# Optimization experiments

Measured on AMD Instinct MI355X. Metric: run time of the kernel, lower is better.

The kernel has to match this reference:

```python
import jax, jax.numpy as jnp
import numpy as np
from jax import lax

B, M, L = 4, 20, 200
IN_C, C1, C2 = 2048, 512, 256
CDIM, DC1, DC2, SDIM = 300, 512, 256, 1024
NEG = -1e15  # -INFINITY in source


def conv1d(x, w, b, pad):
    # x: [N, Cin, L], w: [Cout, Cin, K]
    y = lax.conv_general_dilated(x, w, (1,), ((pad, pad),),
                                 dimension_numbers=('NCH', 'OIH', 'NCH'))
    return y + b[None, :, None]


def maxpool2(x):
    return lax.reduce_window(x, -jnp.inf, lax.max, (1, 1, 2), (1, 1, 2), 'VALID')


def deconv1d(x, w, b):
    # torch ConvTranspose1d(k=4, s=2, p=1): conv with lhs_dilation=2, pad k-1-p=2,
    # kernel flipped and in/out swapped. w: [Cin, Cout, K]
    wt = jnp.flip(w, -1).transpose(1, 0, 2)  # [Cout, Cin, K]
    y = lax.conv_general_dilated(x, wt, (1,), ((2, 2),), lhs_dilation=(2,),
                                 dimension_numbers=('NCH', 'OIH', 'NCH'))
    return y + b[None, :, None]


def setup_inputs() -> dict:
    key = jax.random.key(0)
    ks = jax.random.split(key, 16)
    p = lambda k, sh, s=0.02: (jax.random.normal(k, sh, jnp.float32) * s)
    return dict(
        batch=jax.random.normal(ks[0], (B, M, L, IN_C), jnp.float32),
        seg_len=jax.random.randint(ks[1], (B, M), 1, L + 1, jnp.int32),
        concept1=jax.random.normal(ks[2], (B, CDIM), jnp.float32),
        concept2=jax.random.normal(ks[3], (B, CDIM), jnp.float32),
        w_conv1=p(ks[4], (C1, IN_C, 5)), b_conv1=jnp.zeros((C1,), jnp.float32),
        w_conv2=p(ks[5], (C2, C1, 5)), b_conv2=jnp.zeros((C2,), jnp.float32),
        w_ca1=p(ks[6], (C2, CDIM)), w_ca2=p(ks[7], (C2, C2)), w_ca3=p(ks[8], (1, C2)),
        w_dc1=p(ks[9], (3 * C2, DC1, 4)), b_dc1=jnp.zeros((DC1,), jnp.float32),
        w_dc2=p(ks[10], (DC1, DC2, 4)), b_dc2=jnp.zeros((DC2,), jnp.float32),
        w_sim1=p(ks[11], (SDIM, DC2)), w_sim2=p(ks[12], (SDIM, CDIM)),
        w_mlp=p(ks[13], (1, SDIM)), b_mlp=jnp.zeros((1,), jnp.float32),
    )


def reference(batch, seg_len, concept1, concept2,
              w_conv1, b_conv1, w_conv2, b_conv2,
              w_ca1, w_ca2, w_ca3,
              w_dc1, b_dc1, w_dc2, b_dc2,
              w_sim1, w_sim2, w_mlp, b_mlp):
    Bs, Ms, Ls = batch.shape[:3]
    Lq = Ls // 4
    x = batch.reshape(Bs * Ms, Ls, -1).transpose(0, 2, 1)        # [BM, IN_C, L]
    t1 = maxpool2(conv1d(x, w_conv1, b_conv1, 2))                # [BM, C1, L/2]
    t2 = maxpool2(conv1d(t1, w_conv2, b_conv2, 2)).transpose(0, 2, 1)  # [BM, L/4, C2]

    # vectorized ragged mask: k < ceil(seg_len/4)
    mask = (jnp.arange(Lq)[None, None, :] < ((seg_len + 3) // 4)[:, :, None])
    mask = mask.reshape(Bs * Ms, Lq)

    kproj = t2 @ w_ca2.T                                         # [BM, Lq, C2]

    def concept_att(concept):
        # additive attention; scores are identical across the query-frame dim,
        # so compute one row and broadcast the weighted sum.
        q = concept @ w_ca1.T                                    # [B, C2]
        qe = jnp.repeat(q, Ms, axis=0)                           # [BM, C2]
        s = jnp.tanh(qe[:, None, :] + kproj) @ w_ca3[0]          # [BM, Lq]
        s = jnp.where(mask, s, NEG)
        a = jax.nn.softmax(s, axis=-1)
        r = jnp.einsum('bk,bkc->bc', a, t2)                      # [BM, C2]
        return jnp.broadcast_to(r[:, None, :], t2.shape)         # [BM, Lq, C2]

    r1 = concept_att(concept1)
    r2 = concept_att(concept2)

    cat = jnp.concatenate([t2, r1, r2], axis=-1).transpose(0, 2, 1)  # [BM, 3C2, Lq]
    d = deconv1d(cat, w_dc1, b_dc1)                              # [BM, DC1, L/2]
    d = deconv1d(d, w_dc2, b_dc2).transpose(0, 2, 1)             # [BM, L, DC2]
    d = d.reshape(Bs, Ms * Ls, -1)

    sim1 = d @ w_sim1.T                                          # [B, M*L, SDIM]
    c1 = concept1 @ w_sim2.T                                     # [B, SDIM]
    c2 = concept2 @ w_sim2.T
    sc1 = jax.nn.sigmoid((c1[:, None, :] * sim1) @ w_mlp[0] + b_mlp[0])
    sc2 = jax.nn.sigmoid((c2[:, None, :] * sim1) @ w_mlp[0] + b_mlp[0])
    return sc1.reshape(Bs, Ms, Ls), sc2.reshape(Bs, Ms, Ls)
```

## Files before the change

### kernel.cpp

```cpp
#include <hip/hip_runtime.h>
#include <hip/hip_bf16.h>
#include <math.h>

#define BB 4
#define MM 20
#define LL 200
#define INC 2048
#define C1 512
#define C2 256
#define CDIM 300
#define DC1 512
#define DC2 256
#define SDIM 1024
#define BM 80
#define L2 100
#define L4 50

typedef unsigned short u16;
typedef __attribute__((ext_vector_type(8))) short bf16x8;
typedef __attribute__((ext_vector_type(4))) float f32x4;

__device__ __forceinline__ u16 f2bf_rne(float f) {
  unsigned u = __float_as_uint(f);
  unsigned r = u + 0x7FFFu + ((u >> 16) & 1u);
  return (u16)(r >> 16);
}
__device__ __forceinline__ float bf2f(u16 v) {
  return __uint_as_float(((unsigned)v) << 16);
}

__device__ __forceinline__ void gload16(const u16* g, u16* l) {
  __builtin_amdgcn_global_load_lds(
      (const __attribute__((address_space(1))) void*)g,
      (__attribute__((address_space(3))) void*)l, 16, 0, 0);
}

__global__ void k_cast_pad_batch(const float* __restrict__ in, u16* __restrict__ out) {
  int idx = blockIdx.x * 256 + threadIdx.x;
  if (idx >= 80 * 204 * 256) return;
  int c8 = idx % 256;
  int pi = (idx / 256) % 204;
  int n  = idx / (256 * 204);
  uint4 o = make_uint4(0u, 0u, 0u, 0u);
  if (pi >= 2 && pi < 202) {
    const float* p = in + ((long long)(n * 200 + pi - 2) * 2048 + c8 * 8);
    float4 a = *(const float4*)p;
    float4 b = *(const float4*)(p + 4);
    o.x = (unsigned)f2bf_rne(a.x) | ((unsigned)f2bf_rne(a.y) << 16);
    o.y = (unsigned)f2bf_rne(a.z) | ((unsigned)f2bf_rne(a.w) << 16);
    o.z = (unsigned)f2bf_rne(b.x) | ((unsigned)f2bf_rne(b.y) << 16);
    o.w = (unsigned)f2bf_rne(b.z) | ((unsigned)f2bf_rne(b.w) << 16);
  }
  int key = (n * 204 + pi) & 7;
  long long pos = ((long long)(n * 204 + pi)) * 256 + (c8 ^ key);
  *(uint4*)(out + pos * 8) = o;
}

__global__ void k_zero_pad(u16* __restrict__ p, int ncnt, int rpad, int lr, int P,
                           int cin8, int total) {
  int idx = blockIdx.x * 256 + threadIdx.x;
  if (idx >= total) return;
  int c = idx % cin8;
  int pr = (idx / cin8) % (rpad - lr);
  int n = idx / (cin8 * (rpad - lr));
  int row = (pr < P) ? pr : lr + pr;
  *(uint4*)(p + ((long long)(n * rpad + row) * cin8 + c) * 8) = make_uint4(0, 0, 0, 0);
}

__global__ void k_cast_bf16(const float* __restrict__ in, u16* __restrict__ out, int n8) {
  int idx = blockIdx.x * 256 + threadIdx.x;
  if (idx >= n8) return;
  const float4* p = (const float4*)in + (long long)idx * 2;
  float4 a = p[0], b = p[1];
  uint4 o;
  o.x = (unsigned)f2bf_rne(a.x) | ((unsigned)f2bf_rne(a.y) << 16);
  o.y = (unsigned)f2bf_rne(a.z) | ((unsigned)f2bf_rne(a.w) << 16);
  o.z = (unsigned)f2bf_rne(b.x) | ((unsigned)f2bf_rne(b.y) << 16);
  o.w = (unsigned)f2bf_rne(b.z) | ((unsigned)f2bf_rne(b.w) << 16);
  *(uint4*)(out + (long long)idx * 8) = o;
}

__global__ __launch_bounds__(256) void k_conv_w_lds(
    const float* __restrict__ in, u16* __restrict__ out, int Cin, int Kk) {
  __shared__ u16 l[10240];
  int co = blockIdx.x;
  int n = Cin * Kk;
  int tid = threadIdx.x;
  const float* src = in + (long long)co * n;
  for (int i = tid; i < n; i += 256) l[i] = f2bf_rne(src[i]);
  __syncthreads();
  u16* dst = out + (long long)co * n;
  int n8 = n >> 3;
  for (int j8 = tid; j8 < n8; j8 += 256) {
    int j = j8 * 8;
    int t = j / Cin, ci = j - t * Cin;
    u16 tmp[8];
    #pragma unroll
    for (int e = 0; e < 8; ++e) tmp[e] = l[(ci + e) * Kk + t];
    uint4 o;
    o.x = tmp[0] | ((unsigned)tmp[1] << 16);
    o.y = tmp[2] | ((unsigned)tmp[3] << 16);
    o.z = tmp[4] | ((unsigned)tmp[5] << 16);
    o.w = tmp[6] | ((unsigned)tmp[7] << 16);
    *(uint4*)&dst[j] = o;
  }
}

__global__ __launch_bounds__(256) void k_deconv_w_t(
    const float* __restrict__ in, u16* __restrict__ out, int Cin, int Cout) {
  __shared__ u16 l[64][65];
  int C = Cout * 4;
  int nci = Cin >> 6;
  int ci0 = (blockIdx.x % nci) << 6;
  int c0  = (blockIdx.x / nci) << 6;
  int tid = threadIdx.x;
  int cc = tid & 63, rr = tid >> 6;
  #pragma unroll 4
  for (int p = 0; p < 16; ++p) {
    int r = rr + p * 4;
    l[r][cc] = f2bf_rne(in[(long long)(ci0 + r) * C + c0 + cc]);
  }
  __syncthreads();
  #pragma unroll 4
  for (int p = 0; p < 16; ++p) {
    int cl = rr + p * 4;
    int c = c0 + cl;
    int co = c >> 2, t = c & 3;
    int z = (3 - t) & 1, tt = (3 - t) >> 1;
    out[(((long long)z * Cout + co) * 2 + tt) * Cin + ci0 + cc] = l[cc][cl];
  }
}

__global__ __launch_bounds__(256) void k_prep_small(
    const float* __restrict__ concept1, const float* __restrict__ concept2,
    const float* __restrict__ w_ca1, const float* __restrict__ w_sim1,
    const float* __restrict__ w_sim2, const float* __restrict__ w_mlp,
    float* __restrict__ qv) {
  int cz = blockIdx.x >> 2;
  int b  = blockIdx.x & 3;
  const float* con = cz ? concept2 : concept1;
  __shared__ float cvec[CDIM];
  __shared__ float chat[SDIM];
  int tid = threadIdx.x;
  for (int j = tid; j < CDIM; j += 256) cvec[j] = con[b * CDIM + j];
  __syncthreads();
  float accq = 0.f;
  for (int j = 0; j < CDIM; ++j) accq += cvec[j] * w_ca1[tid * CDIM + j];
  qv[(cz * 4 + b) * 256 + tid] = accq;
  for (int i = 0; i < 4; ++i) {
    int s = tid + i * 256;
    float a2 = 0.f;
    for (int j = 0; j < CDIM; ++j) a2 += cvec[j] * w_sim2[s * CDIM + j];
    chat[s] = a2 * w_mlp[s];
  }
  __syncthreads();
  float v = 0.f;
  for (int s = 0; s < SDIM; ++s) v += w_sim1[s * 256 + tid] * chat[s];
  qv[2048 + (cz * 4 + b) * 256 + tid] = v;
}

template <int SWZO>
__global__ __launch_bounds__(256) void k_gemm_conv(
    const u16* __restrict__ A, const u16* __restrict__ Bw,
    u16* __restrict__ Co, const float* __restrict__ bias,
    int M, int N, int Ktot, int cin, int ncib,
    int lr, int rpad, int px, int yspan, int gy,
    int orpad, int ooff, long long aend) {
  __shared__ __align__(16) u16 At[2][10240];
  __shared__ __align__(16) u16 Bs[2][8192];
  int id = blockIdx.x;
  int k8 = id & 7, j = id >> 3;
  int x = k8 / px, h = k8 - x * px;
  int y = h * yspan + j;
  if (y >= gy) return;
  int row0 = y * 128, col0 = x * 128;
  int tid = threadIdx.x, w = tid >> 6, ln = tid & 63;
  int r15 = ln & 15, q = ln >> 4;

  int n0 = row0 / lr, l0 = row0 - n0 * lr;
  long long prow0 = (long long)n0 * rpad + l0;

  int wrb = (w >> 1) * 64;
  int rlb[4], pp[4];
  #pragma unroll
  for (int mi = 0; mi < 4; ++mi) {
    int rr = wrb + mi * 16 + r15;
    int nc = (row0 + rr) / lr - n0;
    rlb[mi] = rr + 4 * nc;
    pp[mi] = (int)((prow0 + rlb[mi]) & 7);
  }

  long long arow_base = prow0 + w * 40 + (ln >> 3);
  const u16* alim = A + (aend - 8);
  auto stA = [&](int cib_, int pc) {
    const u16* src = A + (arow_base + pc * 8) * cin + cib_ * 64 + (ln & 7) * 8;
    if (src > alim) src = alim;
    gload16(src, At[cib_ & 1] + (w * 40 + pc * 8) * 64);
  };

  const u16* gb[4];
  #pragma unroll
  for (int i = 0; i < 4; ++i) {
    int f = 4 * w + i, blk = f >> 1, ks = f & 1;
    int klocal = ks * 32 + q * 8;
    int br = col0 + blk * 16 + r15;
    gb[i] = Bw + ((long long)br * Ktot + klocal);
  }
  int wbase = 4 * w * 512;

  f32x4 acc[4][4];
  #pragma unroll
  for (int i = 0; i < 4; ++i)
    #pragma unroll
    for (int j2 = 0; j2 < 4; ++j2) acc[i][j2] = (f32x4){0.f, 0.f, 0.f, 0.f};
  int wc2 = (w & 1) * 4;

  #pragma unroll
  for (int pc = 0; pc < 5; ++pc) stA(0, pc);
  #pragma unroll
  for (int i = 0; i < 4; ++i) gload16(gb[i], Bs[0] + wbase + i * 512);
  #pragma unroll
  for (int i = 0; i < 4; ++i) gb[i] += cin;
  int ts = 1;
  asm volatile("s_waitcnt vmcnt(0)" ::: "memory");
  __builtin_amdgcn_s_barrier();

  long long bwrap = 64 - 4 * (long long)cin;
  for (int cib = 0; cib < ncib; ++cib) {
    bool lastcib = (cib == ncib - 1);
    #pragma unroll
    for (int t = 0; t < 5; ++t) {
      bool lastc = lastcib && (t == 4);
      if (!lastcib) stA(cib + 1, t);
      if (!lastc) {
        int bufn = (cib + t + 1) & 1;
        #pragma unroll
        for (int i = 0; i < 4; ++i) gload16(gb[i], Bs[bufn] + wbase + i * 512);
        long long d = (ts == 4) ? bwrap : (long long)cin;
        ts = (ts == 4) ? 0 : ts + 1;
        #pragma unroll
        for (int i = 0; i < 4; ++i) gb[i] += d;
      }
      if (lastc)        asm volatile("s_waitcnt vmcnt(0)" ::: "memory");
      else if (lastcib) asm volatile("s_waitcnt vmcnt(4)" ::: "memory");
      else              asm volatile("s_waitcnt vmcnt(5)" ::: "memory");
      __builtin_amdgcn_s_barrier();
      __builtin_amdgcn_sched_barrier(0);
      const u16* Ab = At[cib & 1];
      const u16* Bb = Bs[(cib + t) & 1];
      int rof[4], pr8[4];
      #pragma unroll
      for (int mi = 0; mi < 4; ++mi) {
        rof[mi] = (rlb[mi] + t) * 64;
        pr8[mi] = (pp[mi] + t) & 7;
      }
      #pragma unroll
      for (int ks = 0; ks < 2; ++ks) {
        bf16x8 af[4], bf[4];
        #pragma unroll
        for (int mi = 0; mi < 4; ++mi)
          af[mi] = *(const bf16x8*)&Ab[rof[mi] + (((ks * 4 + q) ^ pr8[mi]) * 8)];
        #pragma unroll
        for (int ni = 0; ni < 4; ++ni)
          bf[ni] = *(const bf16x8*)&Bb[(((wc2 + ni) * 2 + ks) * 512) + ln * 8];
        #pragma unroll
        for (int mi = 0; mi < 4; ++mi)
          #pragma unroll
          for (int ni = 0; ni < 4; ++ni)
            acc[mi][ni] = __builtin_amdgcn_mfma_f32_16x16x32_bf16(
                af[mi], bf[ni], acc[mi][ni], 0, 0, 0);
      }
      __builtin_amdgcn_sched_barrier(0);
      __builtin_amdgcn_s_barrier();
    }
  }

  int q4 = q * 4;
  int wrow = (w >> 1) * 64, wcol = (w & 1) * 64;
  int lrh = lr >> 1;
  #pragma unroll
  for (int mi = 0; mi < 4; ++mi) {
    int gbase = row0 + wrow + mi * 16 + q4;
    #pragma unroll
    for (int p = 0; p < 2; ++p) {
      int grow = gbase + 2 * p;
      if (grow < M) {
        int prow = grow >> 1;
        int n = prow / lrh, ll = prow - n * lrh;
        long long orow = (long long)n * orpad + ooff + ll;
        int key = SWZO ? ((int)(orow & 7) << 3) : 0;
        #pragma unroll
        for (int ni = 0; ni < 4; ++ni) {
          int col = col0 + wcol + ni * 16 + r15;
          float v = fmaxf(acc[mi][ni][2 * p], acc[mi][ni][2 * p + 1]) + bias[col];
          Co[orow * N + (col ^ key)] = f2bf_rne(v);
        }
      }
    }
  }
}

#define EP_PLAIN 0
#define EP_POOL  1
#define EP_ILV   2

template <int EP>
__global__ __launch_bounds__(256) void k_gemm(
    const u16* __restrict__ A, const u16* __restrict__ Bw,
    void* __restrict__ Co, const float* __restrict__ bias,
    int M, int N, int Ktot, int nchunk,
    int lr, int rpad, int cin, int off0c, int taps,
    int px, int yspan, int gy, long long sB, int orpad, int ooff) {
  __shared__ __align__(16) u16 As[2][8192];
  __shared__ __align__(16) u16 Bs[2][8192];
  int id = blockIdx.x;
  int k8 = id & 7, j = id >> 3;
  int x = k8 / px, h = k8 - x * px;
  int y = h * yspan + j;
  if (y >= gy) return;
  int z = blockIdx.z;
  int off0 = (EP == EP_ILV) ? z : off0c;
  int row0 = y * 128, col0 = x * 128;
  int tid = threadIdx.x, w = tid >> 6, ln = tid & 63;
  const u16* Bz = Bw + (long long)z * sB;

  const u16* ga[4];
  const u16* gb[4];
  #pragma unroll
  for (int i = 0; i < 4; ++i) {
    int f = 4 * w + i, blk = f >> 1, ks = f & 1;
    int klocal = ks * 32 + (ln >> 4) * 8;
    int ar = row0 + blk * 16 + (ln & 15);
    int n_ = ar / lr, l_ = ar - n_ * lr;
    ga[i] = A + ((long long)(n_ * rpad + l_ + off0) * cin + klocal);
    int br = col0 + blk * 16 + (ln & 15);
    gb[i] = Bz + ((long long)br * Ktot + klocal);
  }
  int wbase = 4 * w * 512;

  f32x4 acc[4][4];
  #pragma unroll
  for (int i = 0; i < 4; ++i)
    #pragma unroll
    for (int j2 = 0; j2 < 4; ++j2) acc[i][j2] = (f32x4){0.f, 0.f, 0.f, 0.f};

  int wr2 = (w >> 1) * 4;
  int wc2 = (w & 1) * 4;

  long long dstep = cin;
  long long dwrap = 64 - (long long)(taps - 1) * cin;
  int tc = 0;

  #pragma unroll
  for (int i = 0; i < 4; ++i) {
    gload16(ga[i], As[0] + wbase + i * 512);
    gload16(gb[i], Bs[0] + wbase + i * 512);
  }
  {
    long long d = (tc == taps - 1) ? dwrap : dstep;
    tc = (tc == taps - 1) ? 0 : tc + 1;
    #pragma unroll
    for (int i = 0; i < 4; ++i) { ga[i] += d; gb[i] += d; }
  }

  for (int c = 0; c < nchunk; ++c) {
    int cur = c & 1;
    if (c + 1 < nchunk) {
      u16* dA = As[cur ^ 1] + wbase;
      u16* dB = Bs[cur ^ 1] + wbase;
      #pragma unroll
      for (int i = 0; i < 4; ++i) {
        gload16(ga[i], dA + i * 512);
        gload16(gb[i], dB + i * 512);
      }
      long long d = (tc == taps - 1) ? dwrap : dstep;
      tc = (tc == taps - 1) ? 0 : tc + 1;
      #pragma unroll
      for (int i = 0; i < 4; ++i) { ga[i] += d; gb[i] += d; }
      asm volatile("s_waitcnt vmcnt(8)" ::: "memory");
    } else {
      asm volatile("s_waitcnt vmcnt(0)" ::: "memory");
    }
    __builtin_amdgcn_s_barrier();
    __builtin_amdgcn_sched_barrier(0);
    #pragma unroll
    for (int ks = 0; ks < 2; ++ks) {
      bf16x8 af[4], bf[4];
      #pragma unroll
      for (int mi = 0; mi < 4; ++mi)
        af[mi] = *(const bf16x8*)&As[cur][(((wr2 + mi) * 2 + ks) * 512) + ln * 8];
      #pragma unroll
      for (int ni = 0; ni < 4; ++ni)
        bf[ni] = *(const bf16x8*)&Bs[cur][(((wc2 + ni) * 2 + ks) * 512) + ln * 8];
      #pragma unroll
      for (int mi = 0; mi < 4; ++mi)
        #pragma unroll
        for (int ni = 0; ni < 4; ++ni)
          acc[mi][ni] = __builtin_amdgcn_mfma_f32_16x16x32_bf16(
              af[mi], bf[ni], acc[mi][ni], 0, 0, 0);
    }
    __builtin_amdgcn_sched_barrier(0);
    __builtin_amdgcn_s_barrier();
  }

  int c15 = ln & 15, q4 = (ln >> 4) * 4;
  int wrow = (w >> 1) * 64, wcol = (w & 1) * 64;
  if (EP == EP_PLAIN) {
    float* Cz = (float*)Co;
    #pragma unroll
    for (int mi = 0; mi < 4; ++mi) {
      int gbase = row0 + wrow + mi * 16 + q4;
      #pragma unroll
      for (int r = 0; r < 4; ++r) {
        int grow = gbase + r;
        if (grow < M) {
          #pragma unroll
          for (int ni = 0; ni < 4; ++ni) {
            int col = col0 + wcol + ni * 16 + c15;
            Cz[(long long)grow * N + col] = acc[mi][ni][r];
          }
        }
      }
    }
  } else if (EP == EP_POOL) {
    u16* Cz = (u16*)Co;
    int lrh = lr >> 1;
    #pragma unroll
    for (int mi = 0; mi < 4; ++mi) {
      int gbase = row0 + wrow + mi * 16 + q4;
      #pragma unroll
      for (int p = 0; p < 2; ++p) {
        int grow = gbase + 2 * p;
        if (grow < M) {
          int prow = grow >> 1;
          int n = prow / lrh, ll = prow - n * lrh;
          long long orow = (long long)n * orpad + ooff + ll;
          #pragma unroll
          for (int ni = 0; ni < 4; ++ni) {
            int col = col0 + wcol + ni * 16 + c15;
            float v = fmaxf(acc[mi][ni][2 * p], acc[mi][ni][2 * p + 1]) + bias[col];
            Cz[orow * N + col] = f2bf_rne(v);
          }
        }
      }
    }
  } else {
    u16* Cz = (u16*)Co;
    #pragma unroll
    for (int mi = 0; mi < 4; ++mi) {
      int gbase = row0 + wrow + mi * 16 + q4;
      #pragma unroll
      for (int r = 0; r < 4; ++r) {
        int grow = gbase + r;
        if (grow < M) {
          int n = grow / lr, l = grow - n * lr;
          long long orow = (long long)n * orpad + ooff + 2 * l + z;
          #pragma unroll
          for (int ni = 0; ni < 4; ++ni) {
            int col = col0 + wcol + ni * 16 + c15;
            Cz[orow * N + col] = f2bf_rne(acc[mi][ni][r] + bias[col]);
          }
        }
      }
    }
  }
}

__global__ __launch_bounds__(256) void k_attention(
    const float* __restrict__ kproj, const u16* __restrict__ t2b,
    const float* __restrict__ qv, const float* __restrict__ w_ca3,
    const int* __restrict__ seg_len, u16* __restrict__ rb) {
  int bm = blockIdx.x % BM;
  int cz = blockIdx.x / BM;
  int b = bm / MM;
  int tid = threadIdx.x, w = tid >> 6, ln = tid & 63;
  __shared__ float sq[256], sw[256], sa[L4 + 14];
  sq[tid] = qv[(cz * 4 + b) * 256 + tid];
  sw[tid] = w_ca3[tid];
  __syncthreads();
  int kmax = (seg_len[bm] + 3) >> 2;
  for (int k = w; k < L4; k += 4) {
    float val = 0.f;
    #pragma unroll
    for (int i = 0; i < 4; ++i) {
      int c = ln + 64 * i;
      val += tanhf(sq[c] + kproj[(bm * L4 + k) * 256 + c]) * sw[c];
    }
    for (int off = 32; off > 0; off >>= 1) val += __shfl_down(val, off, 64);
    if (ln == 0) sa[k] = (k < kmax) ? val : -1e15f;
  }
  __syncthreads();
  if (w == 0) {
    float sv = (ln < L4) ? sa[ln] : -3e38f;
    float mx = sv;
    for (int off = 32; off > 0; off >>= 1) mx = fmaxf(mx, __shfl_down(mx, off, 64));
    mx = __shfl(mx, 0, 64);
    float e = (ln < L4) ? expf(sv - mx) : 0.f;
    float s = e;
    for (int off = 32; off > 0; off >>= 1) s += __shfl_down(s, off, 64);
    s = __shfl(s, 0, 64);
    if (ln < L4) sa[ln] = e / s;
  }
  __syncthreads();
  float r = 0.f;
  for (int k = 0; k < L4; ++k) r += sa[k] * bf2f(t2b[(bm * L4 + k) * 256 + tid]);
  rb[(cz * BM + bm) * 256 + tid] = f2bf_rne(r);
}

__global__ void k_build_cat(const u16* __restrict__ t2b, const u16* __restrict__ rb,
                            u16* __restrict__ catm, int total) {
  int idx = blockIdx.x * 256 + threadIdx.x;
  if (idx >= total) return;
  int ci = idx % 768;
  int row = idx / 768;
  int bm = row / L4, li = row - bm * L4;
  u16 v;
  if (ci < 256)      v = t2b[row * 256 + ci];
  else if (ci < 512) v = rb[bm * 256 + (ci - 256)];
  else               v = rb[(BM + bm) * 256 + (ci - 512)];
  catm[((long long)(bm * 52 + 1 + li)) * 768 + ci] = v;
}

__global__ __launch_bounds__(256) void k_final(
    const u16* __restrict__ d2b, const float* __restrict__ qv,
    const float* __restrict__ b_mlp, float* __restrict__ out) {
  int wv = blockIdx.x * 4 + (threadIdx.x >> 6);
  int ln = threadIdx.x & 63;
  int row0 = wv * 16;
  int b = row0 / 4000;
  float4 q1 = *(const float4*)&qv[2048 + b * 256 + ln * 4];
  float4 q2 = *(const float4*)&qv[2048 + 1024 + b * 256 + ln * 4];
  float bmlp = b_mlp[0];
  for (int r = 0; r < 16; ++r) {
    int row = row0 + r;
    ushort4 v = *(const ushort4*)&d2b[(long long)row * 256 + ln * 4];
    float x0 = bf2f(v.x), x1 = bf2f(v.y), x2 = bf2f(v.z), x3 = bf2f(v.w);
    float p1 = x0 * q1.x + x1 * q1.y + x2 * q1.z + x3 * q1.w;
    float p2 = x0 * q2.x + x1 * q2.y + x2 * q2.z + x3 * q2.w;
    for (int off = 32; off > 0; off >>= 1) {
      p1 += __shfl_down(p1, off, 64);
      p2 += __shfl_down(p2, off, 64);
    }
    if (ln == 0) {
      out[row]         = 1.f / (1.f + expf(-(p1 + bmlp)));
      out[16000 + row] = 1.f / (1.f + expf(-(p2 + bmlp)));
    }
  }
}

extern "C" void kernel_launch(void* const* d_in, const int* in_sizes, int n_in,
                              void* d_out, int out_size, void* d_ws, size_t ws_size,
                              hipStream_t stream) {
  const float* batch    = (const float*)d_in[0];
  const int*   seg_len  = (const int*)d_in[1];
  const float* concept1 = (const float*)d_in[2];
  const float* concept2 = (const float*)d_in[3];
  const float* w_conv1  = (const float*)d_in[4];
  const float* b_conv1  = (const float*)d_in[5];
  const float* w_conv2  = (const float*)d_in[6];
  const float* b_conv2  = (const float*)d_in[7];
  const float* w_ca1    = (const float*)d_in[8];
  const float* w_ca2    = (const float*)d_in[9];
  const float* w_ca3    = (const float*)d_in[10];
  const float* w_dc1    = (const float*)d_in[11];
  const float* b_dc1    = (const float*)d_in[12];
  const float* w_dc2    = (const float*)d_in[13];
  const float* b_dc2    = (const float*)d_in[14];
  const float* w_sim1   = (const float*)d_in[15];
  const float* w_sim2   = (const float*)d_in[16];
  const float* w_mlp    = (const float*)d_in[17];
  const float* b_mlp    = (const float*)d_in[18];
  float* out = (float*)d_out;

  float* ws = (float*)d_ws;
  const long long off_qv    = 0;
  const long long off_kproj = 4096;
  const long long off_rb    = 1028096;
  const long long off_t1    = 1048576;
  const long long off_t2    = 3211264;
  const long long off_w1b   = 3735552;
  const long long off_w2b   = 6356992;
  const long long off_wd1p  = 6684672;
  const long long off_wd2p  = 7471104;
  const long long off_wca2b = 7733248;
  const long long off_BIG   = 7766016;

  u16* rb    = (u16*)(ws + off_rb);
  u16* t1b   = (u16*)(ws + off_t1);
  u16* t2b   = (u16*)(ws + off_t2);
  u16* w1b   = (u16*)(ws + off_w1b);
  u16* w2b   = (u16*)(ws + off_w2b);
  u16* wd1p  = (u16*)(ws + off_wd1p);
  u16* wd2p  = (u16*)(ws + off_wd2p);
  u16* wca2b = (u16*)(ws + off_wca2b);
  u16* batchb = (u16*)(ws + off_BIG);
  u16* catm   = (u16*)(ws + off_BIG);
  u16* d1b    = (u16*)(ws + off_BIG) + 3342336;
  u16* d2b    = (u16*)(ws + off_BIG) + 7667712;

  k_cast_pad_batch<<<dim3(16320), 256, 0, stream>>>(batch, batchb);
  k_conv_w_lds<<<dim3(512), 256, 0, stream>>>(w_conv1, w1b, INC, 5);
  k_conv_w_lds<<<dim3(256), 256, 0, stream>>>(w_conv2, w2b, C1, 5);
  k_deconv_w_t<<<dim3(384), 256, 0, stream>>>(w_dc1, wd1p, 3 * C2, DC1);
  k_deconv_w_t<<<dim3(128), 256, 0, stream>>>(w_dc2, wd2p, DC1, DC2);
  k_cast_bf16<<<dim3(32), 256, 0, stream>>>(w_ca2, wca2b, 8192);
  k_prep_small<<<dim3(8), 256, 0, stream>>>(concept1, concept2, w_ca1, w_sim1, w_sim2,
                                            w_mlp, ws + off_qv);
  k_zero_pad<<<dim3(80), 256, 0, stream>>>(t1b, 80, 104, 100, 2, 64, 20480);

  k_gemm_conv<1><<<dim3(504), 256, 0, stream>>>(
      batchb, w1b, t1b, b_conv1, 16000, 512, 10240, 2048, 32,
      200, 204, 2, 63, 125, 104, 2, 80LL * 204 * 2048);

  k_zero_pad<<<dim3(60), 256, 0, stream>>>(catm, 80, 52, 50, 1, 96, 15360);
  k_zero_pad<<<dim3(40), 256, 0, stream>>>(d1b, 80, 102, 100, 1, 64, 10240);

  k_gemm_conv<0><<<dim3(128), 256, 0, stream>>>(
      t1b, w2b, t2b, b_conv2, 8000, 256, 2560, 512, 8,
      100, 104, 4, 16, 63, 50, 0, 80LL * 104 * 512);

  k_gemm<EP_PLAIN><<<dim3(64), 256, 0, stream>>>(
      t2b, wca2b, ws + off_kproj, nullptr, 4000, 256, 256, 4,
      4000, 4000, 256, 0, 1, 4, 8, 32, 0, 0, 0);

  k_attention<<<dim3(160), 256, 0, stream>>>(ws + off_kproj, t2b, ws + off_qv,
                                             w_ca3, seg_len, rb);

  k_build_cat<<<dim3(12000), 256, 0, stream>>>(t2b, rb, catm, 4000 * 768);

  k_gemm<EP_ILV><<<dim3(128, 1, 2), 256, 0, stream>>>(
      catm, wd1p, d1b, b_dc1, 4000, 512, 1536, 24,
      50, 52, 768, 0, 2, 2, 16, 32, 786432LL, 102, 1);

  k_gemm<EP_ILV><<<dim3(128, 1, 2), 256, 0, stream>>>(
      d1b, wd2p, d2b, b_dc2, 8000, 256, 1024, 16,
      100, 102, 512, 0, 2, 4, 16, 63, 262144LL, 200, 0);

  k_final<<<dim3(250), 256, 0, stream>>>(d2b, ws + off_qv, b_mlp, out);
}
```

Baseline: 733.6 us.

## Merge prep kernels into one launch, combine zero-pads, vectorize cat build

Folds the batch cast/pad, conv and deconv weight repacks, w_ca2 cast, concept precompute and t1 zero-padding into a single block-dispatched kernel. The two later zero-pad launches become one, and the concat builder now moves 16-byte chunks instead of single bf16 elements. GEMM templates are wrapped in named kernels and the unused pool epilogue is removed. The aim is to cut launch count and the gaps between launches, at the cost of a larger kernel whose shared-memory and register use is sized for its heaviest branch.

```diff
diff --git a/kernel.cpp b/kernel.cpp
--- a/kernel.cpp
+++ b/kernel.cpp
@@ -35,132 +35,147 @@
       (__attribute__((address_space(3))) void*)l, 16, 0, 0);
 }
 
-__global__ void k_cast_pad_batch(const float* __restrict__ in, u16* __restrict__ out) {
-  int idx = blockIdx.x * 256 + threadIdx.x;
-  if (idx >= 80 * 204 * 256) return;
-  int c8 = idx % 256;
-  int pi = (idx / 256) % 204;
-  int n  = idx / (256 * 204);
-  uint4 o = make_uint4(0u, 0u, 0u, 0u);
-  if (pi >= 2 && pi < 202) {
-    const float* p = in + ((long long)(n * 200 + pi - 2) * 2048 + c8 * 8);
-    float4 a = *(const float4*)p;
-    float4 b = *(const float4*)(p + 4);
+__global__ __launch_bounds__(256) void k_prep_all(
+    const float* __restrict__ batch, const float* __restrict__ w_conv1,
+    const float* __restrict__ w_conv2, const float* __restrict__ w_dc1,
+    const float* __restrict__ w_dc2, const float* __restrict__ w_ca2,
+    const float* __restrict__ concept1, const float* __restrict__ concept2,
+    const float* __restrict__ w_ca1, const float* __restrict__ w_sim1,
+    const float* __restrict__ w_sim2, const float* __restrict__ w_mlp,
+    u16* __restrict__ batchb, u16* __restrict__ w1b, u16* __restrict__ w2b,
+    u16* __restrict__ wd1p, u16* __restrict__ wd2p, u16* __restrict__ wca2b,
+    float* __restrict__ qv, u16* __restrict__ t1b) {
+  __shared__ __align__(16) u16 sh[10240];
+  int bid = blockIdx.x;
+  int tid = threadIdx.x;
+
+  if (bid < 16320) {
+    int idx = bid * 256 + tid;
+    int c8 = idx % 256;
+    int pi = (idx / 256) % 204;
+    int n  = idx / (256 * 204);
+    uint4 o = make_uint4(0u, 0u, 0u, 0u);
+    if (pi >= 2 && pi < 202) {
+      const float* p = batch + ((long long)(n * 200 + pi - 2) * 2048 + c8 * 8);
+      float4 a = *(const float4*)p;
+      float4 b = *(const float4*)(p + 4);
+      o.x = (unsigned)f2bf_rne(a.x) | ((unsigned)f2bf_rne(a.y) << 16);
+      o.y = (unsigned)f2bf_rne(a.z) | ((unsigned)f2bf_rne(a.w) << 16);
+      o.z = (unsigned)f2bf_rne(b.x) | ((unsigned)f2bf_rne(b.y) << 16);
+      o.w = (unsigned)f2bf_rne(b.z) | ((unsigned)f2bf_rne(b.w) << 16);
+    }
+    int key = (n * 204 + pi) & 7;
+    long long pos = ((long long)(n * 204 + pi)) * 256 + (c8 ^ key);
+    *(uint4*)(batchb + pos * 8) = o;
+  } else if (bid < 17088) {
+    const float* in; u16* out; int Cin, co;
+    if (bid < 16832) { in = w_conv1; out = w1b; Cin = INC; co = bid - 16320; }
+    else             { in = w_conv2; out = w2b; Cin = C1;  co = bid - 16832; }
+    int n = Cin * 5;
+    const float* src = in + (long long)co * n;
+    for (int i = tid; i < n; i += 256) sh[i] = f2bf_rne(src[i]);
+    __syncthreads();
+    u16* dst = out + (long long)co * n;
+    int n8 = n >> 3;
+    for (int j8 = tid; j8 < n8; j8 += 256) {
+      int j = j8 * 8;
+      int t = j / Cin, ci = j - t * Cin;
+      u16 tmp[8];
+      #pragma unroll
+      for (int e = 0; e < 8; ++e) tmp[e] = sh[(ci + e) * 5 + t];
+      uint4 o;
+      o.x = tmp[0] | ((unsigned)tmp[1] << 16);
+      o.y = tmp[2] | ((unsigned)tmp[3] << 16);
+      o.z = tmp[4] | ((unsigned)tmp[5] << 16);
+      o.w = tmp[6] | ((unsigned)tmp[7] << 16);
+      *(uint4*)&dst[j] = o;
+    }
+  } else if (bid < 17600) {
+    u16 (*l)[65] = (u16(*)[65])sh;
+    const float* in; u16* out; int Cin, Cout, b2;
+    if (bid < 17472) { in = w_dc1; out = wd1p; Cin = 3 * C2; Cout = DC1; b2 = bid - 17088; }
+    else             { in = w_dc2; out = wd2p; Cin = DC1;    Cout = DC2; b2 = bid - 17472; }
+    int C = Cout * 4;
+    int nci = Cin >> 6;
+    int ci0 = (b2 % nci) << 6;
+    int c0  = (b2 / nci) << 6;
+    int cc = tid & 63, rr = tid >> 6;
+    #pragma unroll 4
+    for (int p = 0; p < 16; ++p) {
+      int r = rr + p * 4;
+      l[r][cc] = f2bf_rne(in[(long long)(ci0 + r) * C + c0 + cc]);
+    }
+    __syncthreads();
+    #pragma unroll 4
+    for (int p = 0; p < 16; ++p) {
+      int cl = rr + p * 4;
+      int c = c0 + cl;
+      int co = c >> 2, t = c & 3;
+      int z = (3 - t) & 1, tt = (3 - t) >> 1;
+      out[(((long long)z * Cout + co) * 2 + tt) * Cin + ci0 + cc] = l[cc][cl];
+    }
+  } else if (bid < 17632) {
+    int idx = (bid - 17600) * 256 + tid;
+    const float4* p = (const float4*)w_ca2 + (long long)idx * 2;
+    float4 a = p[0], b = p[1];
+    uint4 o;
     o.x = (unsigned)f2bf_rne(a.x) | ((unsigned)f2bf_rne(a.y) << 16);
     o.y = (unsigned)f2bf_rne(a.z) | ((unsigned)f2bf_rne(a.w) << 16);
     o.z = (unsigned)f2bf_rne(b.x) | ((unsigned)f2bf_rne(b.y) << 16);
     o.w = (unsigned)f2bf_rne(b.z) | ((unsigned)f2bf_rne(b.w) << 16);
-  }
-  int key = (n * 204 + pi) & 7;
-  long long pos = ((long long)(n * 204 + pi)) * 256 + (c8 ^ key);
-  *(uint4*)(out + pos * 8) = o;
-}
-
-__global__ void k_zero_pad(u16* __restrict__ p, int ncnt, int rpad, int lr, int P,
-                           int cin8, int total) {
+    *(uint4*)(wca2b + (long long)idx * 8) = o;
+  } else if (bid < 17640) {
+    float* cvec = (float*)sh;
+    float* chat = (float*)sh + 320;
+    int b2 = bid - 17632;
+    int cz = b2 >> 2;
+    int b  = b2 & 3;
+    const float* con = cz ? concept2 : concept1;
+    for (int j = tid; j < CDIM; j += 256) cvec[j] = con[b * CDIM + j];
+    __syncthreads();
+    float accq = 0.f;
+    for (int j = 0; j < CDIM; ++j) accq += cvec[j] * w_ca1[tid * CDIM + j];
+    qv[(cz * 4 + b) * 256 + tid] = accq;
+    for (int i = 0; i < 4; ++i) {
+      int s = tid + i * 256;
+      float a2 = 0.f;
+      for (int j = 0; j < CDIM; ++j) a2 += cvec[j] * w_sim2[s * CDIM + j];
+      chat[s] = a2 * w_mlp[s];
+    }
+    __syncthreads();
+    float v = 0.f;
+    for (int s = 0; s < SDIM; ++s) v += w_sim1[s * 256 + tid] * chat[s];
+    qv[2048 + (cz * 4 + b) * 256 + tid] = v;
+  } else {
+    int idx = (bid - 17640) * 256 + tid;
+    int c = idx % 64;
+    int pr = (idx / 64) % 4;
+    int n = idx / 256;
+    int row = (pr < 2) ? pr : 100 + pr;
+    *(uint4*)(t1b + ((long long)(n * 104 + row) * 64 + c) * 8) = make_uint4(0, 0, 0, 0);
+  }
+}
+
+__global__ void k_zero_pad2(u16* __restrict__ catm, u16* __restrict__ d1b) {
   int idx = blockIdx.x * 256 + threadIdx.x;
-  if (idx >= total) return;
-  int c = idx % cin8;
-  int pr = (idx / cin8) % (rpad - lr);
-  int n = idx / (cin8 * (rpad - lr));
-  int row = (pr < P) ? pr : lr + pr;
-  *(uint4*)(p + ((long long)(n * rpad + row) * cin8 + c) * 8) = make_uint4(0, 0, 0, 0);
-}
-
-__global__ void k_cast_bf16(const float* __restrict__ in, u16* __restrict__ out, int n8) {
-  int idx = blockIdx.x * 256 + threadIdx.x;
-  if (idx >= n8) return;
-  const float4* p = (const float4*)in + (long long)idx * 2;
-  float4 a = p[0], b = p[1];
-  uint4 o;
-  o.x = (unsigned)f2bf_rne(a.x) | ((unsigned)f2bf_rne(a.y) << 16);
-  o.y = (unsigned)f2bf_rne(a.z) | ((unsigned)f2bf_rne(a.w) << 16);
-  o.z = (unsigned)f2bf_rne(b.x) | ((unsigned)f2bf_rne(b.y) << 16);
-  o.w = (unsigned)f2bf_rne(b.z) | ((unsigned)f2bf_rne(b.w) << 16);
-  *(uint4*)(out + (long long)idx * 8) = o;
-}
-
-__global__ __launch_bounds__(256) void k_conv_w_lds(
-    const float* __restrict__ in, u16* __restrict__ out, int Cin, int Kk) {
-  __shared__ u16 l[10240];
-  int co = blockIdx.x;
-  int n = Cin * Kk;
-  int tid = threadIdx.x;
-  const float* src = in + (long long)co * n;
-  for (int i = tid; i < n; i += 256) l[i] = f2bf_rne(src[i]);
-  __syncthreads();
-  u16* dst = out + (long long)co * n;
-  int n8 = n >> 3;
-  for (int j8 = tid; j8 < n8; j8 += 256) {
-    int j = j8 * 8;
-    int t = j / Cin, ci = j - t * Cin;
-    u16 tmp[8];
-    #pragma unroll
-    for (int e = 0; e < 8; ++e) tmp[e] = l[(ci + e) * Kk + t];
-    uint4 o;
-    o.x = tmp[0] | ((unsigned)tmp[1] << 16);
-    o.y = tmp[2] | ((unsigned)tmp[3] << 16);
-    o.z = tmp[4] | ((unsigned)tmp[5] << 16);
-    o.w = tmp[6] | ((unsigned)tmp[7] << 16);
-    *(uint4*)&dst[j] = o;
-  }
-}
-
-__global__ __launch_bounds__(256) void k_deconv_w_t(
-    const float* __restrict__ in, u16* __restrict__ out, int Cin, int Cout) {
-  __shared__ u16 l[64][65];
-  int C = Cout * 4;
-  int nci = Cin >> 6;
-  int ci0 = (blockIdx.x % nci) << 6;
-  int c0  = (blockIdx.x / nci) << 6;
-  int tid = threadIdx.x;
-  int cc = tid & 63, rr = tid >> 6;
-  #pragma unroll 4
-  for (int p = 0; p < 16; ++p) {
-    int r = rr + p * 4;
-    l[r][cc] = f2bf_rne(in[(long long)(ci0 + r) * C + c0 + cc]);
-  }
-  __syncthreads();
-  #pragma unroll 4
-  for (int p = 0; p < 16; ++p) {
-    int cl = rr + p * 4;
-    int c = c0 + cl;
-    int co = c >> 2, t = c & 3;
-    int z = (3 - t) & 1, tt = (3 - t) >> 1;
-    out[(((long long)z * Cout + co) * 2 + tt) * Cin + ci0 + cc] = l[cc][cl];
-  }
-}
-
-__global__ __launch_bounds__(256) void k_prep_small(
-    const float* __restrict__ concept1, const float* __restrict__ concept2,
-    const float* __restrict__ w_ca1, const float* __restrict__ w_sim1,
-    const float* __restrict__ w_sim2, const float* __restrict__ w_mlp,
-    float* __restrict__ qv) {
-  int cz = blockIdx.x >> 2;
-  int b  = blockIdx.x & 3;
-  const float* con = cz ? concept2 : concept1;
-  __shared__ float cvec[CDIM];
-  __shared__ float chat[SDIM];
-  int tid = threadIdx.x;
-  for (int j = tid; j < CDIM; j += 256) cvec[j] = con[b * CDIM + j];
-  __syncthreads();
-  float accq = 0.f;
-  for (int j = 0; j < CDIM; ++j) accq += cvec[j] * w_ca1[tid * CDIM + j];
-  qv[(cz * 4 + b) * 256 + tid] = accq;
-  for (int i = 0; i < 4; ++i) {
-    int s = tid + i * 256;
-    float a2 = 0.f;
-    for (int j = 0; j < CDIM; ++j) a2 += cvec[j] * w_sim2[s * CDIM + j];
-    chat[s] = a2 * w_mlp[s];
-  }
-  __syncthreads();
-  float v = 0.f;
-  for (int s = 0; s < SDIM; ++s) v += w_sim1[s * 256 + tid] * chat[s];
-  qv[2048 + (cz * 4 + b) * 256 + tid] = v;
+  if (idx < 15360) {
+    int c = idx % 96;
+    int pr = (idx / 96) & 1;
+    int n = idx / 192;
+    int row = pr ? 51 : 0;
+    *(uint4*)(catm + ((long long)(n * 52 + row) * 96 + c) * 8) = make_uint4(0, 0, 0, 0);
+  } else {
+    int j = idx - 15360;
+    int c = j % 64;
+    int pr = (j / 64) & 1;
+    int n = j / 128;
+    int row = pr ? 101 : 0;
+    *(uint4*)(d1b + ((long long)(n * 102 + row) * 64 + c) * 8) = make_uint4(0, 0, 0, 0);
+  }
 }
 
 template <int SWZO>
-__global__ __launch_bounds__(256) void k_gemm_conv(
+__device__ __forceinline__ void gemm_conv_body(
     const u16* __restrict__ A, const u16* __restrict__ Bw,
     u16* __restrict__ Co, const float* __restrict__ bias,
     int M, int N, int Ktot, int cin, int ncib,
@@ -300,12 +315,29 @@
   }
 }
 
+__global__ __launch_bounds__(256) void k_conv1_gemm(
+    const u16* __restrict__ A, const u16* __restrict__ Bw,
+    u16* __restrict__ Co, const float* __restrict__ bias,
+    int M, int N, int Ktot, int cin, int ncib, int lr, int rpad,
+    int px, int yspan, int gy, int orpad, int ooff, long long aend) {
+  gemm_conv_body<1>(A, Bw, Co, bias, M, N, Ktot, cin, ncib, lr, rpad,
+                    px, yspan, gy, orpad, ooff, aend);
+}
+__global__ __launch_bounds__(256) void k_conv2_gemm(
+    const u16* __restrict__ A, const u16* __restrict__ Bw,
+    u16* __restrict__ Co, const float* __restrict__ bias,
+    int M, int N, int Ktot, int cin, int ncib, int lr, int rpad,
+    int px, int yspan, int gy, int orpad, int ooff, long long aend) {
+  gemm_conv_body<0>(A, Bw, Co, bias, M, N, Ktot, cin, ncib, lr, rpad,
+                    px, yspan, gy, orpad, ooff, aend);
+}
+
 #define EP_PLAIN 0
 #define EP_POOL  1
 #define EP_ILV   2
 
 template <int EP>
-__global__ __launch_bounds__(256) void k_gemm(
+__device__ __forceinline__ void gemm_body(
     const u16* __restrict__ A, const u16* __restrict__ Bw,
     void* __restrict__ Co, const float* __restrict__ bias,
     int M, int N, int Ktot, int nchunk,
@@ -422,28 +454,6 @@
         }
       }
     }
-  } else if (EP == EP_POOL) {
-    u16* Cz = (u16*)Co;
-    int lrh = lr >> 1;
-    #pragma unroll
-    for (int mi = 0; mi < 4; ++mi) {
-      int gbase = row0 + wrow + mi * 16 + q4;
-      #pragma unroll
-      for (int p = 0; p < 2; ++p) {
-        int grow = gbase + 2 * p;
-        if (grow < M) {
-          int prow = grow >> 1;
-          int n = prow / lrh, ll = prow - n * lrh;
-          long long orow = (long long)n * orpad + ooff + ll;
-          #pragma unroll
-          for (int ni = 0; ni < 4; ++ni) {
-            int col = col0 + wcol + ni * 16 + c15;
-            float v = fmaxf(acc[mi][ni][2 * p], acc[mi][ni][2 * p + 1]) + bias[col];
-            Cz[orow * N + col] = f2bf_rne(v);
-          }
-        }
-      }
-    }
   } else {
     u16* Cz = (u16*)Co;
     #pragma unroll
@@ -464,6 +474,31 @@
       }
     }
   }
+}
+
+__global__ __launch_bounds__(256) void k_kproj_gemm(
+    const u16* __restrict__ A, const u16* __restrict__ Bw,
+    void* __restrict__ Co, const float* __restrict__ bias,
+    int M, int N, int Ktot, int nchunk, int lr, int rpad, int cin, int off0c,
+    int taps, int px, int yspan, int gy, long long sB, int orpad, int ooff) {
+  gemm_body<EP_PLAIN>(A, Bw, Co, bias, M, N, Ktot, nchunk, lr, rpad, cin, off0c,
+                      taps, px, yspan, gy, sB, orpad, ooff);
+}
+__global__ __launch_bounds__(256) void k_dc1_gemm(
+    const u16* __restrict__ A, const u16* __restrict__ Bw,
+    void* __restrict__ Co, const float* __restrict__ bias,
+    int M, int N, int Ktot, int nchunk, int lr, int rpad, int cin, int off0c,
+    int taps, int px, int yspan, int gy, long long sB, int orpad, int ooff) {
+  gemm_body<EP_ILV>(A, Bw, Co, bias, M, N, Ktot, nchunk, lr, rpad, cin, off0c,
+                    taps, px, yspan, gy, sB, orpad, ooff);
+}
+__global__ __launch_bounds__(256) void k_dc2_gemm(
+    const u16* __restrict__ A, const u16* __restrict__ Bw,
+    void* __restrict__ Co, const float* __restrict__ bias,
+    int M, int N, int Ktot, int nchunk, int lr, int rpad, int cin, int off0c,
+    int taps, int px, int yspan, int gy, long long sB, int orpad, int ooff) {
+  gemm_body<EP_ILV>(A, Bw, Co, bias, M, N, Ktot, nchunk, lr, rpad, cin, off0c,
+                    taps, px, yspan, gy, sB, orpad, ooff);
 }
 
 __global__ __launch_bounds__(256) void k_attention(
@@ -508,17 +543,16 @@
 }
 
 __global__ void k_build_cat(const u16* __restrict__ t2b, const u16* __restrict__ rb,
-                            u16* __restrict__ catm, int total) {
+                            u16* __restrict__ catm) {
   int idx = blockIdx.x * 256 + threadIdx.x;
-  if (idx >= total) return;
-  int ci = idx % 768;
-  int row = idx / 768;
+  int u = idx % 96;
+  int row = idx / 96;
   int bm = row / L4, li = row - bm * L4;
-  u16 v;
-  if (ci < 256)      v = t2b[row * 256 + ci];
-  else if (ci < 512) v = rb[bm * 256 + (ci - 256)];
-  else               v = rb[(BM + bm) * 256 + (ci - 512)];
-  catm[((long long)(bm * 52 + 1 + li)) * 768 + ci] = v;
+  uint4 v;
+  if (u < 32)      v = *(const uint4*)&t2b[row * 256 + u * 8];
+  else if (u < 64) v = *(const uint4*)&rb[bm * 256 + (u - 32) * 8];
+  else             v = *(const uint4*)&rb[(BM + bm) * 256 + (u - 64) * 8];
+  *(uint4*)&catm[((long long)(bm * 52 + 1 + li)) * 768 + u * 8] = v;
 }
 
 __global__ __launch_bounds__(256) void k_final(
@@ -598,41 +632,35 @@
   u16* d1b    = (u16*)(ws + off_BIG) + 3342336;
   u16* d2b    = (u16*)(ws + off_BIG) + 7667712;
 
-  k_cast_pad_batch<<<dim3(16320), 256, 0, stream>>>(batch, batchb);
-  k_conv_w_lds<<<dim3(512), 256, 0, stream>>>(w_conv1, w1b, INC, 5);
-  k_conv_w_lds<<<dim3(256), 256, 0, stream>>>(w_conv2, w2b, C1, 5);
-  k_deconv_w_t<<<dim3(384), 256, 0, stream>>>(w_dc1, wd1p, 3 * C2, DC1);
-  k_deconv_w_t<<<dim3(128), 256, 0, stream>>>(w_dc2, wd2p, DC1, DC2);
-  k_cast_bf16<<<dim3(32), 256, 0, stream>>>(w_ca2, wca2b, 8192);
-  k_prep_small<<<dim3(8), 256, 0, stream>>>(concept1, concept2, w_ca1, w_sim1, w_sim2,
-                                            w_mlp, ws + off_qv);
-  k_zero_pad<<<dim3(80), 256, 0, stream>>>(t1b, 80, 104, 100, 2, 64, 20480);
-
-  k_gemm_conv<1><<<dim3(504), 256, 0, stream>>>(
+  k_prep_all<<<dim3(17720), 256, 0, stream>>>(
+      batch, w_conv1, w_conv2, w_dc1, w_dc2, w_ca2,
+      concept1, concept2, w_ca1, w_sim1, w_sim2, w_mlp,
+      batchb, w1b, w2b, wd1p, wd2p, wca2b, ws + off_qv, t1b);
+
+  k_conv1_gemm<<<dim3(504), 256, 0, stream>>>(
       batchb, w1b, t1b, b_conv1, 16000, 512, 10240, 2048, 32,
       200, 204, 2, 63, 125, 104, 2, 80LL * 204 * 2048);
 
-  k_zero_pad<<<dim3(60), 256, 0, stream>>>(catm, 80, 52, 50, 1, 96, 15360);
-  k_zero_pad<<<dim3(40), 256, 0, stream>>>(d1b, 80, 102, 100, 1, 64, 10240);
-
-  k_gemm_conv<0><<<dim3(128), 256, 0, stream>>>(
+  k_zero_pad2<<<dim3(100), 256, 0, stream>>>(catm, d1b);
+
+  k_conv2_gemm<<<dim3(128), 256, 0, stream>>>(
       t1b, w2b, t2b, b_conv2, 8000, 256, 2560, 512, 8,
       100, 104, 4, 16, 63, 50, 0, 80LL * 104 * 512);
 
-  k_gemm<EP_PLAIN><<<dim3(64), 256, 0, stream>>>(
+  k_kproj_gemm<<<dim3(64), 256, 0, stream>>>(
       t2b, wca2b, ws + off_kproj, nullptr, 4000, 256, 256, 4,
       4000, 4000, 256, 0, 1, 4, 8, 32, 0, 0, 0);
 
   k_attention<<<dim3(160), 256, 0, stream>>>(ws + off_kproj, t2b, ws + off_qv,
                                              w_ca3, seg_len, rb);
 
-  k_build_cat<<<dim3(12000), 256, 0, stream>>>(t2b, rb, catm, 4000 * 768);
-
-  k_gemm<EP_ILV><<<dim3(128, 1, 2), 256, 0, stream>>>(
+  k_build_cat<<<dim3(1500), 256, 0, stream>>>(t2b, rb, catm);
+
+  k_dc1_gemm<<<dim3(128, 1, 2), 256, 0, stream>>>(
       catm, wd1p, d1b, b_dc1, 4000, 512, 1536, 24,
       50, 52, 768, 0, 2, 2, 16, 32, 786432LL, 102, 1);
 
-  k_gemm<EP_ILV><<<dim3(128, 1, 2), 256, 0, stream>>>(
+  k_dc2_gemm<<<dim3(128, 1, 2), 256, 0, stream>>>(
       d1b, wd2p, d2b, b_dc2, 8000, 256, 1024, 16,
       100, 102, 512, 0, 2, 4, 16, 63, 262144LL, 200, 0);
 
```

Measured after the change: 872.7 us. 19.0% more time.
